# Kernel optimization log

Hardware: AMD Instinct MI355X
Metric: run time of the kernel (lower is better)

## Reference

```python
import jax, jax.numpy as jnp
import numpy as np

D_IN = 1024
D_OUT = 1024
NUM_HEADS = 16
HEAD_DIM = D_OUT // NUM_HEADS
CONTEXT_LEN = 2048


def setup_inputs() -> dict:
    key = jax.random.key(0)
    ks = jax.random.split(key, 7)
    scale = 0.02
    x = jax.random.normal(ks[0], (2, 2048, D_IN), dtype=jnp.float32)
    Wq = jax.random.normal(ks[1], (D_IN, D_OUT), dtype=jnp.float32) * scale
    bq = jnp.zeros((D_OUT,), dtype=jnp.float32)
    Wk = jax.random.normal(ks[2], (D_IN, D_OUT), dtype=jnp.float32) * scale
    bk = jnp.zeros((D_OUT,), dtype=jnp.float32)
    Wv = jax.random.normal(ks[3], (D_IN, D_OUT), dtype=jnp.float32) * scale
    bv = jnp.zeros((D_OUT,), dtype=jnp.float32)
    return {"x": x, "Wq": Wq, "bq": bq, "Wk": Wk, "bk": bk, "Wv": Wv, "bv": bv}


def reference(x, Wq, bq, Wk, bk, Wv, bv):
    B, S, _ = x.shape
    # QKV projections with bias
    q = x @ Wq + bq  # [B,S,D_OUT]
    k = x @ Wk + bk
    v = x @ Wv + bv
    # split heads -> [B,H,S,Dh]
    def heads(t):
        return t.reshape(B, S, NUM_HEADS, HEAD_DIM).transpose(0, 2, 1, 3)
    q, k, v = heads(q), heads(k), heads(v)
    # raw scores, then additive causal mask (-1e9 on strictly upper triangle),
    # then scale by 1/sqrt(head_dim) AFTER adding mask (matches original code)
    scores = jnp.einsum("bhqd,bhkd->bhqk", q, k)
    causal = jnp.tril(jnp.ones((S, S), dtype=bool))
    add_mask = jnp.where(causal, 0.0, -1e9).astype(scores.dtype)
    scores = scores + add_mask
    weights = jax.nn.softmax(scores / jnp.sqrt(jnp.asarray(HEAD_DIM, scores.dtype)), axis=-1)
    ctx = jnp.einsum("bhqk,bhkd->bhqd", weights, v)  # [B,H,S,Dh]
    return ctx.transpose(0, 2, 1, 3).reshape(B, S, D_OUT)
```

## Files before the change

kernel.cpp:

```cpp
#include <hip/hip_runtime.h>
#include <hip/hip_bf16.h>
#include <stdint.h>

#define D_IN 1024
#define NH 16
#define DH 64
#define SEQ 2048
#define BATCH 2

typedef unsigned short u16;
typedef __attribute__((ext_vector_type(8))) short short8;
typedef __attribute__((ext_vector_type(4))) float f32x4;

#define CSCALE 0.1803368801f

__device__ __forceinline__ u16 f2bf(float f) {
    union { float f; uint32_t u; } v; v.f = f;
    uint32_t r = v.u + 0x7FFF + ((v.u >> 16) & 1);
    return (u16)(r >> 16);
}

__device__ __forceinline__ uint32_t pktrunc(float a, float b) {
    union { float f; uint32_t u; } x, y;
    x.f = a; y.f = b;
    return __builtin_amdgcn_perm(y.u, x.u, 0x07060302u);
}

__device__ __forceinline__ void async16(const u16* g, u16* l) {
    __builtin_amdgcn_global_load_lds(
        (const __attribute__((address_space(1))) void*)g,
        (__attribute__((address_space(3))) void*)l, 16, 0, 0);
}

__global__ __launch_bounds__(256) void prep_kernel(
    const float* __restrict__ x, const float* __restrict__ Wq,
    const float* __restrict__ Wk, const float* __restrict__ Wv,
    u16* __restrict__ xb, u16* __restrict__ WT)
{
    __shared__ float tile[64][65];
    if (blockIdx.x < 4096) {
        int i = (blockIdx.x * 256 + threadIdx.x) * 4;
        float4 v = *(const float4*)(x + i);
        union { u16 u[4]; uint2 d; } o;
        o.u[0] = f2bf(v.x); o.u[1] = f2bf(v.y); o.u[2] = f2bf(v.z); o.u[3] = f2bf(v.w);
        *(uint2*)(xb + i) = o.d;
        return;
    }
    int idx = blockIdx.x - 4096;
    int mat = idx >> 8, rem = idx & 255;
    int k0 = (rem & 15) * 64, n0 = (rem >> 4) * 64;
    const float* W = (mat == 0) ? Wq : (mat == 1 ? Wk : Wv);
    int c = threadIdx.x & 63, rb = threadIdx.x >> 6;
    #pragma unroll
    for (int p = 0; p < 16; ++p) {
        int r = p * 4 + rb;
        tile[r][c] = W[(size_t)(k0 + r) * 1024 + n0 + c];
    }
    __syncthreads();
    #pragma unroll
    for (int p = 0; p < 16; ++p) {
        int r = p * 4 + rb;
        WT[((size_t)mat * 1024 + n0 + r) * 1024 + k0 + c] = f2bf(tile[c][r]);
    }
}

__global__ __launch_bounds__(256) void qkv_gemm_kernel(
    const u16* __restrict__ xb, const u16* __restrict__ WT,
    const float* __restrict__ bq, const float* __restrict__ bk,
    const float* __restrict__ bv,
    u16* __restrict__ Qb, u16* __restrict__ Kb, u16* __restrict__ Vh)
{
    __shared__ u16 As[128 * 32];
    __shared__ u16 Bs[128 * 32];
    const int tid  = threadIdx.x;
    const int wave = tid >> 6, lane = tid & 63;
    const int quad = lane >> 4, l15 = lane & 15;
    const int m0 = blockIdx.y * 128;
    const int n0 = blockIdx.x * 128;

    f32x4 acc[4][4];
    #pragma unroll
    for (int i = 0; i < 4; ++i)
        #pragma unroll
        for (int j = 0; j < 4; ++j)
            acc[i][j] = (f32x4){0.f, 0.f, 0.f, 0.f};

    const int wm = wave & 1, wn = wave >> 1;
    const int srow = wave * 32 + (lane >> 2);
    const int scol = (lane & 3) * 8;

    for (int k0 = 0; k0 < 1024; k0 += 32) {
        #pragma unroll
        for (int t = 0; t < 2; ++t) {
            int row = srow + t * 16;
            async16(xb + (size_t)(m0 + row) * 1024 + k0 + scol, As + row * 32 + scol);
            async16(WT + (size_t)(n0 + row) * 1024 + k0 + scol, Bs + row * 32 + scol);
        }
        __syncthreads();
        short8 af[4], bfr[4];
        #pragma unroll
        for (int f = 0; f < 4; ++f) {
            af[f]  = *(const short8*)(As + (wm * 64 + f * 16 + l15) * 32 + quad * 8);
            bfr[f] = *(const short8*)(Bs + (wn * 64 + f * 16 + l15) * 32 + quad * 8);
        }
        #pragma unroll
        for (int i = 0; i < 4; ++i)
            #pragma unroll
            for (int j = 0; j < 4; ++j)
                acc[i][j] = __builtin_amdgcn_mfma_f32_16x16x32_bf16(af[i], bfr[j], acc[i][j], 0, 0, 0);
        __syncthreads();
    }

    const int mat = n0 >> 10;
    const float* bias = (mat == 0) ? bq : (mat == 1 ? bk : bv);
    u16* dst = (mat == 0) ? Qb : (mat == 1 ? Kb : Vh);
    const float sc = (mat == 0) ? CSCALE : 1.0f;
    const int ncb = (n0 & 1023) + wn * 64;
    const int hh = ncb >> 6;
    #pragma unroll
    for (int i = 0; i < 4; ++i) {
        int gm = m0 + wm * 64 + i * 16 + quad * 4;
        int bb = gm >> 11, ss = gm & 2047;
        #pragma unroll
        for (int j = 0; j < 4; ++j) {
            int dh = j * 16 + l15;
            float bval = bias[ncb + dh];
            size_t base = (((size_t)bb * NH + hh) * SEQ + ss) * DH + dh;
            #pragma unroll
            for (int r = 0; r < 4; ++r)
                dst[base + (size_t)r * DH] = f2bf((acc[i][j][r] + bval) * sc);
        }
    }
}

__global__ __launch_bounds__(256) void transpose_v_kernel(
    const u16* __restrict__ Vh, u16* __restrict__ Vt)
{
    __shared__ uint32_t tile[64][65];
    int s0 = blockIdx.x * 64;
    size_t bh = blockIdx.y;
    int c = threadIdx.x & 63, rb = threadIdx.x >> 6;
    const u16* src = Vh + (bh * SEQ + s0) * DH;
    #pragma unroll
    for (int p = 0; p < 16; ++p) {
        int r = p * 4 + rb;
        tile[r][c] = src[(size_t)r * DH + c];
    }
    __syncthreads();
    u16* dst = Vt + bh * DH * SEQ + s0;
    #pragma unroll
    for (int p = 0; p < 16; ++p) {
        int d = p * 4 + rb;
        dst[(size_t)d * SEQ + c] = (u16)tile[c][d];
    }
}

__device__ __forceinline__ void stage64(const u16* g0, size_t gstride, u16* lds,
                                        int wave, int lane)
{
    #pragma unroll
    for (int rnd = 0; rnd < 2; ++rnd) {
        int row = rnd * 32 + wave * 8 + (lane >> 3);
        int c = (lane & 7) ^ (row & 7);
        async16(g0 + (size_t)row * gstride + c * 8, lds + row * 64 + (lane & 7) * 8);
    }
}

__global__ __launch_bounds__(256) void flash_mfma_kernel(
    const u16* __restrict__ Qb, const u16* __restrict__ Kb,
    const u16* __restrict__ Vt, float* __restrict__ out)
{
    __shared__ u16 Ks[2][64 * 64];
    __shared__ u16 Vs[2][64 * 64];
    __shared__ u16 Ps[128 * 72];

    const int tid  = threadIdx.x;
    const int wave = tid >> 6, lane = tid & 63;
    const int quad = lane >> 4, l15 = lane & 15;
    const int qt = (gridDim.x - 1) - blockIdx.x;
    const int h = blockIdx.y, b = blockIdx.z;
    const int q0 = qt * 128;
    const int wq0 = wave * 32;
    const size_t bh = (size_t)b * NH + h;
    const u16* Qp = Qb + bh * SEQ * DH;
    const u16* Kp = Kb + bh * SEQ * DH;
    const u16* Vp = Vt + bh * DH * SEQ;

    short8 qf[2][2];
    #pragma unroll
    for (int qa = 0; qa < 2; ++qa) {
        const u16* qrp = Qp + (size_t)(q0 + wq0 + qa * 16 + l15) * DH;
        qf[qa][0] = *(const short8*)(qrp + quad * 8);
        qf[qa][1] = *(const short8*)(qrp + 32 + quad * 8);
    }

    f32x4 O[2][4];
    #pragma unroll
    for (int pa = 0; pa < 2; ++pa)
        #pragma unroll
        for (int f = 0; f < 4; ++f) O[pa][f] = (f32x4){0.f, 0.f, 0.f, 0.f};
    float lsum[2] = {0.f, 0.f};

    const int ntiles = 2 * qt + 2;
    const int wqmax = q0 + wq0 + 31;

    stage64(Kp, DH, Ks[0], wave, lane);
    stage64(Vp, SEQ, Vs[0], wave, lane);
    __syncthreads();

    const int xq = l15 & 7;

    for (int t = 0; t < ntiles; ++t) {
        const int cur = t & 1;
        if (t + 1 < ntiles) {
            int k1 = (t + 1) * 64;
            stage64(Kp + (size_t)k1 * DH, DH, Ks[cur ^ 1], wave, lane);
            stage64(Vp + k1, SEQ, Vs[cur ^ 1], wave, lane);
        }
        const int k0 = t * 64;
        if (k0 <= wqmax) {
            f32x4 sf[4][2];
            #pragma unroll
            for (int fj = 0; fj < 4; ++fj) {
                const u16* krow = &Ks[cur][(fj * 16 + l15) * 64];
                short8 k0f = *(const short8*)(krow + (quad ^ xq) * 8);
                short8 k1f = *(const short8*)(krow + ((4 + quad) ^ xq) * 8);
                #pragma unroll
                for (int qa = 0; qa < 2; ++qa) {
                    f32x4 s = (f32x4){0.f, 0.f, 0.f, 0.f};
                    s = __builtin_amdgcn_mfma_f32_16x16x32_bf16(k0f, qf[qa][0], s, 0, 0, 0);
                    s = __builtin_amdgcn_mfma_f32_16x16x32_bf16(k1f, qf[qa][1], s, 0, 0, 0);
                    sf[fj][qa] = s;
                }
            }
            const bool diag = (k0 + 63 > q0 + wq0);
            #pragma unroll
            for (int fj = 0; fj < 4; ++fj)
                #pragma unroll
                for (int qa = 0; qa < 2; ++qa)
                    #pragma unroll
                    for (int r = 0; r < 4; ++r) {
                        float p = __builtin_amdgcn_exp2f(sf[fj][qa][r]);
                        if (diag) {
                            int key = k0 + fj * 16 + quad * 4 + r;
                            int qg  = q0 + wq0 + qa * 16 + l15;
                            p = (key <= qg) ? p : 0.f;
                        }
                        sf[fj][qa][r] = p;
                        lsum[qa] += p;
                    }
            #pragma unroll
            for (int qa = 0; qa < 2; ++qa) {
                u16* prow = &Ps[(wq0 + qa * 16 + l15) * 72];
                #pragma unroll
                for (int fj = 0; fj < 4; ++fj) {
                    uint2 d;
                    d.x = pktrunc(sf[fj][qa][0], sf[fj][qa][1]);
                    d.y = pktrunc(sf[fj][qa][2], sf[fj][qa][3]);
                    *(uint2*)(prow + fj * 16 + quad * 4) = d;
                }
            }
            short8 pfr[2][2];
            #pragma unroll
            for (int pa = 0; pa < 2; ++pa) {
                const u16* prow = &Ps[(wq0 + pa * 16 + l15) * 72];
                pfr[pa][0] = *(const short8*)(prow + quad * 8);
                pfr[pa][1] = *(const short8*)(prow + 32 + quad * 8);
            }
            #pragma unroll
            for (int fo = 0; fo < 4; ++fo) {
                const u16* vrow = &Vs[cur][(fo * 16 + l15) * 64];
                short8 vb0 = *(const short8*)(vrow + (quad ^ xq) * 8);
                short8 vb1 = *(const short8*)(vrow + ((4 + quad) ^ xq) * 8);
                #pragma unroll
                for (int pa = 0; pa < 2; ++pa) {
                    O[pa][fo] = __builtin_amdgcn_mfma_f32_16x16x32_bf16(pfr[pa][0], vb0, O[pa][fo], 0, 0, 0);
                    O[pa][fo] = __builtin_amdgcn_mfma_f32_16x16x32_bf16(pfr[pa][1], vb1, O[pa][fo], 0, 0, 0);
                }
            }
        }
        __syncthreads();
    }

    #pragma unroll
    for (int qa = 0; qa < 2; ++qa) {
        float s = lsum[qa];
        s += __shfl_xor(s, 16);
        s += __shfl_xor(s, 32);
        lsum[qa] = s;
    }
    #pragma unroll
    for (int pa = 0; pa < 2; ++pa)
        #pragma unroll
        for (int fo = 0; fo < 4; ++fo)
            #pragma unroll
            for (int r = 0; r < 4; ++r) {
                float lq = __shfl(lsum[pa], quad * 4 + r);
                int s = q0 + wq0 + pa * 16 + quad * 4 + r;
                out[((size_t)b * SEQ + s) * 1024 + h * DH + fo * 16 + l15] = O[pa][fo][r] / lq;
            }
}

extern "C" void kernel_launch(void* const* d_in, const int* in_sizes, int n_in,
                              void* d_out, int out_size, void* d_ws, size_t ws_size,
                              hipStream_t stream) {
    const float* x  = (const float*)d_in[0];
    const float* Wq = (const float*)d_in[1];
    const float* bq = (const float*)d_in[2];
    const float* Wk = (const float*)d_in[3];
    const float* bk = (const float*)d_in[4];
    const float* Wv = (const float*)d_in[5];
    const float* bv = (const float*)d_in[6];
    float* out = (float*)d_out;

    const size_t NX = (size_t)BATCH * SEQ * D_IN;
    const size_t NW = (size_t)3 * D_IN * 1024;
    const size_t NP = (size_t)BATCH * NH * SEQ * DH;
    u16* xb = (u16*)d_ws;
    u16* WT = xb + NX;
    u16* Qb = WT + NW;
    u16* Kb = Qb + NP;
    u16* Vh = Kb + NP;
    u16* Vt = Vh + NP;

    prep_kernel<<<4096 + 768, 256, 0, stream>>>(x, Wq, Wk, Wv, xb, WT);
    qkv_gemm_kernel<<<dim3(24, 32), 256, 0, stream>>>(xb, WT, bq, bk, bv, Qb, Kb, Vh);
    transpose_v_kernel<<<dim3(SEQ / 64, BATCH * NH), 256, 0, stream>>>(Vh, Vt);
    flash_mfma_kernel<<<dim3(SEQ / 128, NH, BATCH), 256, 0, stream>>>(Qb, Kb, Vt, out);
}
```

Measured before the change: 188.7 us.

## Split long causal query tiles across two blocks and merge partials in combine kernel

The flash kernel grid becomes 32 (batch*head) by 24 jobs: the eight heaviest query tiles (qt 8-15) are split into two halves over the key range, and light tiles (qt 0-7) are paired into single jobs ordered to balance work across the grid. Partial unnormalized outputs (bf16) and row sums go to workspace (reusing the xb buffer), and a new combine kernel adds the halves and normalizes. Row sums are now computed with an MFMA against a ones vector instead of scalar adds plus shuffles, and the P LDS row stride changes from 72 to 76. This trades an extra launch, extra global traffic and bf16 rounding of partial outputs for better load balance of the causal triangle.

```diff
diff --git a/kernel.cpp b/kernel.cpp
--- a/kernel.cpp
+++ b/kernel.cpp
@@ -18,6 +18,11 @@
     union { float f; uint32_t u; } v; v.f = f;
     uint32_t r = v.u + 0x7FFF + ((v.u >> 16) & 1);
     return (u16)(r >> 16);
+}
+
+__device__ __forceinline__ float bf2f(u16 u) {
+    union { uint32_t u; float f; } v; v.u = (uint32_t)u << 16;
+    return v.f;
 }
 
 __device__ __forceinline__ uint32_t pktrunc(float a, float b) {
@@ -168,20 +173,30 @@
 
 __global__ __launch_bounds__(256) void flash_mfma_kernel(
     const u16* __restrict__ Qb, const u16* __restrict__ Kb,
-    const u16* __restrict__ Vt, float* __restrict__ out)
-{
+    const u16* __restrict__ Vt, float* __restrict__ out,
+    u16* __restrict__ Opart, float* __restrict__ Lpart)
+{
+    static const int JQT[24] = {7,15,15,14,14, 6,13,13,12,12, 5,11,11,10,10,
+                                4, 9, 9, 8, 8, 3, 2, 1, 0};
+    static const int JHF[24] = {-1,0,1,0,1, -1,0,1,0,1, -1,0,1,0,1,
+                                -1,0,1,0,1, -1,-1,-1,-1};
+
     __shared__ u16 Ks[2][64 * 64];
     __shared__ u16 Vs[2][64 * 64];
-    __shared__ u16 Ps[128 * 72];
+    __shared__ u16 Ps[128 * 76];
 
     const int tid  = threadIdx.x;
     const int wave = tid >> 6, lane = tid & 63;
     const int quad = lane >> 4, l15 = lane & 15;
-    const int qt = (gridDim.x - 1) - blockIdx.x;
-    const int h = blockIdx.y, b = blockIdx.z;
+    const int bhx = blockIdx.x;
+    const int b = bhx >> 4, h = bhx & 15;
+    const int job = blockIdx.y;
+    const int qt = JQT[job], hf = JHF[job];
+    const int t0 = (hf == 1) ? qt + 1 : 0;
+    const int t1 = (hf == 0) ? qt + 1 : 2 * qt + 2;
     const int q0 = qt * 128;
     const int wq0 = wave * 32;
-    const size_t bh = (size_t)b * NH + h;
+    const size_t bh = (size_t)bhx;
     const u16* Qp = Qb + bh * SEQ * DH;
     const u16* Kp = Kb + bh * SEQ * DH;
     const u16* Vp = Vt + bh * DH * SEQ;
@@ -194,25 +209,27 @@
         qf[qa][1] = *(const short8*)(qrp + 32 + quad * 8);
     }
 
-    f32x4 O[2][4];
-    #pragma unroll
-    for (int pa = 0; pa < 2; ++pa)
+    const short8 ones = (short8){0x3F80, 0x3F80, 0x3F80, 0x3F80,
+                                 0x3F80, 0x3F80, 0x3F80, 0x3F80};
+
+    f32x4 O[2][4], L[2];
+    #pragma unroll
+    for (int pa = 0; pa < 2; ++pa) {
         #pragma unroll
         for (int f = 0; f < 4; ++f) O[pa][f] = (f32x4){0.f, 0.f, 0.f, 0.f};
-    float lsum[2] = {0.f, 0.f};
-
-    const int ntiles = 2 * qt + 2;
+        L[pa] = (f32x4){0.f, 0.f, 0.f, 0.f};
+    }
+
     const int wqmax = q0 + wq0 + 31;
-
-    stage64(Kp, DH, Ks[0], wave, lane);
-    stage64(Vp, SEQ, Vs[0], wave, lane);
+    const int xq = l15 & 7;
+
+    stage64(Kp + (size_t)t0 * 64 * DH, DH, Ks[t0 & 1], wave, lane);
+    stage64(Vp + t0 * 64, SEQ, Vs[t0 & 1], wave, lane);
     __syncthreads();
 
-    const int xq = l15 & 7;
-
-    for (int t = 0; t < ntiles; ++t) {
+    for (int t = t0; t < t1; ++t) {
         const int cur = t & 1;
-        if (t + 1 < ntiles) {
+        if (t + 1 < t1) {
             int k1 = (t + 1) * 64;
             stage64(Kp + (size_t)k1 * DH, DH, Ks[cur ^ 1], wave, lane);
             stage64(Vp + k1, SEQ, Vs[cur ^ 1], wave, lane);
@@ -247,11 +264,10 @@
                             p = (key <= qg) ? p : 0.f;
                         }
                         sf[fj][qa][r] = p;
-                        lsum[qa] += p;
                     }
             #pragma unroll
             for (int qa = 0; qa < 2; ++qa) {
-                u16* prow = &Ps[(wq0 + qa * 16 + l15) * 72];
+                u16* prow = &Ps[(wq0 + qa * 16 + l15) * 76];
                 #pragma unroll
                 for (int fj = 0; fj < 4; ++fj) {
                     uint2 d;
@@ -263,9 +279,14 @@
             short8 pfr[2][2];
             #pragma unroll
             for (int pa = 0; pa < 2; ++pa) {
-                const u16* prow = &Ps[(wq0 + pa * 16 + l15) * 72];
+                const u16* prow = &Ps[(wq0 + pa * 16 + l15) * 76];
                 pfr[pa][0] = *(const short8*)(prow + quad * 8);
                 pfr[pa][1] = *(const short8*)(prow + 32 + quad * 8);
+            }
+            #pragma unroll
+            for (int pa = 0; pa < 2; ++pa) {
+                L[pa] = __builtin_amdgcn_mfma_f32_16x16x32_bf16(pfr[pa][0], ones, L[pa], 0, 0, 0);
+                L[pa] = __builtin_amdgcn_mfma_f32_16x16x32_bf16(pfr[pa][1], ones, L[pa], 0, 0, 0);
             }
             #pragma unroll
             for (int fo = 0; fo < 4; ++fo) {
@@ -282,23 +303,67 @@
         __syncthreads();
     }
 
-    #pragma unroll
-    for (int qa = 0; qa < 2; ++qa) {
-        float s = lsum[qa];
-        s += __shfl_xor(s, 16);
-        s += __shfl_xor(s, 32);
-        lsum[qa] = s;
-    }
-    #pragma unroll
-    for (int pa = 0; pa < 2; ++pa)
-        #pragma unroll
-        for (int fo = 0; fo < 4; ++fo)
-            #pragma unroll
-            for (int r = 0; r < 4; ++r) {
-                float lq = __shfl(lsum[pa], quad * 4 + r);
-                int s = q0 + wq0 + pa * 16 + quad * 4 + r;
-                out[((size_t)b * SEQ + s) * 1024 + h * DH + fo * 16 + l15] = O[pa][fo][r] / lq;
-            }
+    if (hf < 0) {
+        #pragma unroll
+        for (int pa = 0; pa < 2; ++pa)
+            #pragma unroll
+            for (int fo = 0; fo < 4; ++fo)
+                #pragma unroll
+                for (int r = 0; r < 4; ++r) {
+                    int s = q0 + wq0 + pa * 16 + quad * 4 + r;
+                    out[((size_t)b * SEQ + s) * 1024 + h * DH + fo * 16 + l15] =
+                        O[pa][fo][r] / L[pa][r];
+                }
+    } else {
+        const int pi = (qt - 8) * 2 + hf;
+        u16* op = Opart + (((size_t)pi * 32 + bhx) * 128) * 64;
+        float* lp = Lpart + ((size_t)pi * 32 + bhx) * 128;
+        #pragma unroll
+        for (int pa = 0; pa < 2; ++pa) {
+            #pragma unroll
+            for (int fo = 0; fo < 4; ++fo)
+                #pragma unroll
+                for (int r = 0; r < 4; ++r) {
+                    int ql = wq0 + pa * 16 + quad * 4 + r;
+                    op[(size_t)ql * 64 + fo * 16 + l15] = f2bf(O[pa][fo][r]);
+                }
+            if (l15 == 0) {
+                #pragma unroll
+                for (int r = 0; r < 4; ++r)
+                    lp[wq0 + pa * 16 + quad * 4 + r] = L[pa][r];
+            }
+        }
+    }
+}
+
+__global__ __launch_bounds__(256) void combine_kernel(
+    const u16* __restrict__ Opart, const float* __restrict__ Lpart,
+    float* __restrict__ out)
+{
+    int blk = blockIdx.x;
+    int qt = 8 + (blk >> 5);
+    int bh = blk & 31;
+    int b = bh >> 4, h = bh & 15;
+    int pi0 = (qt - 8) * 2, pi1 = pi0 + 1;
+    int tid = threadIdx.x;
+    int q = tid >> 1, seg = (tid & 1) * 32;
+    const u16* o0 = Opart + (((size_t)pi0 * 32 + bh) * 128 + q) * 64 + seg;
+    const u16* o1 = Opart + (((size_t)pi1 * 32 + bh) * 128 + q) * 64 + seg;
+    float inv = 1.0f / (Lpart[((size_t)pi0 * 32 + bh) * 128 + q] +
+                        Lpart[((size_t)pi1 * 32 + bh) * 128 + q]);
+    float* op = out + ((size_t)b * SEQ + qt * 128 + q) * 1024 + h * DH + seg;
+    #pragma unroll
+    for (int d = 0; d < 32; d += 4) {
+        union { uint2 d2; u16 u[4]; } a, c;
+        a.d2 = *(const uint2*)(o0 + d);
+        c.d2 = *(const uint2*)(o1 + d);
+        float4 v;
+        v.x = (bf2f(a.u[0]) + bf2f(c.u[0])) * inv;
+        v.y = (bf2f(a.u[1]) + bf2f(c.u[1])) * inv;
+        v.z = (bf2f(a.u[2]) + bf2f(c.u[2])) * inv;
+        v.w = (bf2f(a.u[3]) + bf2f(c.u[3])) * inv;
+        *(float4*)(op + d) = v;
+    }
 }
 
 extern "C" void kernel_launch(void* const* d_in, const int* in_sizes, int n_in,
@@ -322,9 +387,12 @@
     u16* Kb = Qb + NP;
     u16* Vh = Kb + NP;
     u16* Vt = Vh + NP;
+    u16* Opart = xb;
+    float* Lpart = (float*)(xb + NX);
 
     prep_kernel<<<4096 + 768, 256, 0, stream>>>(x, Wq, Wk, Wv, xb, WT);
     qkv_gemm_kernel<<<dim3(24, 32), 256, 0, stream>>>(xb, WT, bq, bk, bv, Qb, Kb, Vh);
     transpose_v_kernel<<<dim3(SEQ / 64, BATCH * NH), 256, 0, stream>>>(Vh, Vt);
-    flash_mfma_kernel<<<dim3(SEQ / 128, NH, BATCH), 256, 0, stream>>>(Qb, Kb, Vt, out);
-}
+    flash_mfma_kernel<<<dim3(32, 24), 256, 0, stream>>>(Qb, Kb, Vt, out, Opart, Lpart);
+    combine_kernel<<<256, 256, 0, stream>>>(Opart, Lpart, out);
+}
```

New measurement: 170.8 us. -9.5%, faster.
